# Kernel tuning notes

Measured on AMD Instinct MI355X. Metric: run time of the kernel, lower is better.

## Reference

```python
import jax, jax.numpy as jnp
import numpy as np

N_DOMAINS = 8
BATCH, SEQ, VOCAB = 4, 2048, 32000


def setup_inputs() -> dict:
    key = jax.random.key(0)
    k1, k2, k3 = jax.random.split(key, 3)
    sharded_logits = jax.random.normal(k1, (BATCH, SEQ, VOCAB), dtype=jnp.float32)
    label_ids = jax.random.randint(k2, (BATCH, SEQ), 0, VOCAB, dtype=jnp.int64)
    label_mask = jnp.ones((BATCH, SEQ), dtype=bool)
    domain_idxs = jax.random.randint(k3, (BATCH,), 0, N_DOMAINS, dtype=jnp.int64)
    return {"sharded_logits": sharded_logits, "label_ids": label_ids,
            "label_mask": label_mask, "domain_idxs": domain_idxs}


def reference(sharded_logits, label_ids, label_mask, domain_idxs):
    # sharded_cross_entropy(dtype=float): per-token -log p(label), computed in fp32
    logp = jax.nn.log_softmax(sharded_logits.astype(jnp.float32), axis=-1)
    per_token_loss = -jnp.take_along_axis(logp, label_ids[..., None], axis=-1)[..., 0]  # [B, S]

    # masked_mean
    mask = label_mask.astype(jnp.float32)
    ce_loss = jnp.sum(per_token_loss * mask) / jnp.sum(mask)

    # per-domain loss: vectorized segment-sum replaces the python for-loop scatter-add
    per_sample_loss = per_token_loss.sum(axis=-1)                                  # [B]
    domain_losses = jax.ops.segment_sum(per_sample_loss, domain_idxs,
                                        num_segments=N_DOMAINS)                    # [D]
    samples_per_domain = jnp.bincount(domain_idxs, length=N_DOMAINS)               # [D]
    seq_len = per_token_loss.shape[1]
    denom = (samples_per_domain * seq_len).astype(jnp.float32)
    # divide then zero-out NaNs (empty domains) == torch's isnan -> 0 fixup
    normalized = jnp.where(denom > 0, domain_losses / jnp.maximum(denom, 1.0), 0.0)
    return ce_loss, normalized, samples_per_domain
```

## Files before the change

### kernel.cpp

```cpp
#include <hip/hip_runtime.h>
#include <hip/hip_bf16.h>
#include <math.h>


#define NDOM 8

typedef float v4f __attribute__((ext_vector_type(4)));
typedef int   v4i __attribute__((ext_vector_type(4)));

__global__ __launch_bounds__(256) void ce_per_token_kernel(
    const float* __restrict__ logits,
    const int* __restrict__ labels,
    float* __restrict__ per_token_loss,
    int V)
{
    const int token = blockIdx.x;
    const int t = threadIdx.x;
    const v4f* row = reinterpret_cast<const v4f*>(logits + (size_t)token * (size_t)V);
    const int V4 = V >> 2;
    const float L2E = 1.4426950408889634f;
    const float LN2 = 0.6931471805599453f;

    float m[4]  = {-INFINITY, -INFINITY, -INFINITY, -INFINITY};
    float mL[4] = {0.f, 0.f, 0.f, 0.f};
    float s[4]  = {0.f, 0.f, 0.f, 0.f};

    auto upd = [&](int k, v4f v) {
        float m4 = fmaxf(fmaxf(v.x, v.y), fmaxf(v.z, v.w));
        if (m4 > m[k]) {
            s[k] *= exp2f((m[k] - m4) * L2E);
            m[k] = m4;
            mL[k] = m4 * L2E;
        }
        s[k] += exp2f(fmaf(v.x, L2E, -mL[k])) + exp2f(fmaf(v.y, L2E, -mL[k]))
              + exp2f(fmaf(v.z, L2E, -mL[k])) + exp2f(fmaf(v.w, L2E, -mL[k]));
    };

    int j = t;
    for (; j + 768 < V4; j += 1024) {
        v4f v0 = __builtin_nontemporal_load(row + j);
        v4f v1 = __builtin_nontemporal_load(row + j + 256);
        v4f v2 = __builtin_nontemporal_load(row + j + 512);
        v4f v3 = __builtin_nontemporal_load(row + j + 768);
        upd(0, v0); upd(1, v1); upd(2, v2); upd(3, v3);
    }
    for (; j < V4; j += 256) {
        v4f v = __builtin_nontemporal_load(row + j);
        upd(0, v);
    }

    float M = m[0], S = s[0];
    #pragma unroll
    for (int k = 1; k < 4; k++) {
        float mn = fmaxf(M, m[k]);
        S = S * exp2f((M - mn) * L2E) + s[k] * exp2f((m[k] - mn) * L2E);
        M = mn;
    }

    #pragma unroll
    for (int off = 1; off < 64; off <<= 1) {
        float mo = __shfl_xor(M, off, 64);
        float so = __shfl_xor(S, off, 64);
        float mn = fmaxf(M, mo);
        S = S * exp2f((M - mn) * L2E) + so * exp2f((mo - mn) * L2E);
        M = mn;
    }

    __shared__ float sm[4];
    __shared__ float ss[4];
    const int wave = t >> 6;
    if ((t & 63) == 0) { sm[wave] = M; ss[wave] = S; }
    __syncthreads();

    if (t == 0) {
        float Mf = fmaxf(fmaxf(sm[0], sm[1]), fmaxf(sm[2], sm[3]));
        float Sf = ss[0] * exp2f((sm[0] - Mf) * L2E) + ss[1] * exp2f((sm[1] - Mf) * L2E)
                 + ss[2] * exp2f((sm[2] - Mf) * L2E) + ss[3] * exp2f((sm[3] - Mf) * L2E);
        int lab = labels[token];
        float x = logits[(size_t)token * (size_t)V + (size_t)lab];
        per_token_loss[token] = Mf + log2f(Sf) * LN2 - x;
    }
}

__global__ __launch_bounds__(256) void ce_finalize_kernel(
    const float* __restrict__ per_token_loss,
    const int* __restrict__ mask,
    const int* __restrict__ domain_idxs,
    float* __restrict__ out,
    int T, int B, int S)
{
    const int t = threadIdx.x;
    const v4f* pl4 = reinterpret_cast<const v4f*>(per_token_loss);
    const v4i* mk4 = reinterpret_cast<const v4i*>(mask);
    const int T4 = T >> 2;
    const int S4 = S >> 2;

    float tot = 0.0f, cnt = 0.0f;
    float samp[4] = {0.f, 0.f, 0.f, 0.f};

    for (int i = t; i < T4; i += 256) {
        v4f l = pl4[i];
        v4i mk = mk4[i];
        tot += (mk.x ? l.x : 0.f) + (mk.y ? l.y : 0.f)
             + (mk.z ? l.z : 0.f) + (mk.w ? l.w : 0.f);
        cnt += (mk.x ? 1.f : 0.f) + (mk.y ? 1.f : 0.f)
             + (mk.z ? 1.f : 0.f) + (mk.w ? 1.f : 0.f);
        samp[i / S4] += l.x + l.y + l.z + l.w;
    }

    __shared__ float red[6][256];
    red[0][t] = tot;     red[1][t] = cnt;
    red[2][t] = samp[0]; red[3][t] = samp[1];
    red[4][t] = samp[2]; red[5][t] = samp[3];
    __syncthreads();

    for (int off = 128; off > 0; off >>= 1) {
        if (t < off) {
            #pragma unroll
            for (int k = 0; k < 6; k++) red[k][t] += red[k][t + off];
        }
        __syncthreads();
    }

    if (t == 0) {
        out[0] = red[0][0] / red[1][0];

        float dl[NDOM];
        int sc[NDOM];
        #pragma unroll
        for (int d = 0; d < NDOM; d++) { dl[d] = 0.0f; sc[d] = 0; }
        for (int b = 0; b < B; b++) {
            int d = domain_idxs[b];
            dl[d] += red[2 + b][0];
            sc[d] += 1;
        }
        #pragma unroll
        for (int d = 0; d < NDOM; d++) {
            float denom = (float)sc[d] * (float)S;
            out[1 + d]        = (denom > 0.0f) ? (dl[d] / denom) : 0.0f;
            out[1 + NDOM + d] = (float)sc[d];
        }
    }
}

extern "C" void kernel_launch(void* const* d_in, const int* in_sizes, int n_in,
                              void* d_out, int out_size, void* d_ws, size_t ws_size,
                              hipStream_t stream) {
    const float* logits     = (const float*)d_in[0];
    const int* labels       = (const int*)d_in[1];
    const int* mask         = (const int*)d_in[2];
    const int* domain_idxs  = (const int*)d_in[3];
    float* out              = (float*)d_out;

    const int T = in_sizes[1];
    const int V = in_sizes[0] / T;
    const int B = in_sizes[3];
    const int S = T / B;

    float* per_token_loss = (float*)d_ws;

    ce_per_token_kernel<<<T, 256, 0, stream>>>(logits, labels, per_token_loss, V);
    ce_finalize_kernel<<<1, 256, 0, stream>>>(per_token_loss, mask, domain_idxs,
                                              out, T, B, S);
}
```

Before: 1.261 ms.

## Assign one wave per row with register double-buffered loads

```diff
diff --git a/kernel.cpp b/kernel.cpp
--- a/kernel.cpp
+++ b/kernel.cpp
@@ -1,5 +1,4 @@
 #include <hip/hip_runtime.h>
-#include <hip/hip_bf16.h>
 #include <math.h>
 
 
@@ -8,22 +7,30 @@
 typedef float v4f __attribute__((ext_vector_type(4)));
 typedef int   v4i __attribute__((ext_vector_type(4)));
 
-__global__ __launch_bounds__(256) void ce_per_token_kernel(
+__global__ __launch_bounds__(256) void ce_rowwave_kernel(
     const float* __restrict__ logits,
     const int* __restrict__ labels,
     float* __restrict__ per_token_loss,
     int V)
 {
-    const int token = blockIdx.x;
-    const int t = threadIdx.x;
-    const v4f* row = reinterpret_cast<const v4f*>(logits + (size_t)token * (size_t)V);
-    const int V4 = V >> 2;
+    const int lane = threadIdx.x & 63;
+    const int row  = (blockIdx.x << 2) + (threadIdx.x >> 6);
+
     const float L2E = 1.4426950408889634f;
     const float LN2 = 0.6931471805599453f;
 
-    float m[4]  = {-INFINITY, -INFINITY, -INFINITY, -INFINITY};
-    float mL[4] = {0.f, 0.f, 0.f, 0.f};
-    float s[4]  = {0.f, 0.f, 0.f, 0.f};
+    const size_t rowbase = (size_t)row * (size_t)V;
+    const v4f* rp = reinterpret_cast<const v4f*>(logits + rowbase);
+    const int V4     = V >> 2;
+    const int nchunk = V4 >> 6;
+    const int nfull  = nchunk / 5;
+
+    const int   lab = labels[row];
+    const float xl  = logits[rowbase + (size_t)lab];
+
+    float m[5]  = {-INFINITY, -INFINITY, -INFINITY, -INFINITY, -INFINITY};
+    float mL[5] = {0.f, 0.f, 0.f, 0.f, 0.f};
+    float s[5]  = {0.f, 0.f, 0.f, 0.f, 0.f};
 
     auto upd = [&](int k, v4f v) {
         float m4 = fmaxf(fmaxf(v.x, v.y), fmaxf(v.z, v.w));
@@ -36,22 +43,33 @@
               + exp2f(fmaf(v.z, L2E, -mL[k])) + exp2f(fmaf(v.w, L2E, -mL[k]));
     };
 
-    int j = t;
-    for (; j + 768 < V4; j += 1024) {
-        v4f v0 = __builtin_nontemporal_load(row + j);
-        v4f v1 = __builtin_nontemporal_load(row + j + 256);
-        v4f v2 = __builtin_nontemporal_load(row + j + 512);
-        v4f v3 = __builtin_nontemporal_load(row + j + 768);
-        upd(0, v0); upd(1, v1); upd(2, v2); upd(3, v3);
+    v4f cur[5], nxt[5];
+    #pragma unroll
+    for (int c = 0; c < 5; ++c)
+        cur[c] = __builtin_nontemporal_load(rp + (c << 6) + lane);
+
+    for (int i = 1; i < nfull; ++i) {
+        const int base = i * 320 + lane;
+        #pragma unroll
+        for (int c = 0; c < 5; ++c)
+            nxt[c] = __builtin_nontemporal_load(rp + base + (c << 6));
+        #pragma unroll
+        for (int c = 0; c < 5; ++c)
+            upd(c, cur[c]);
+        #pragma unroll
+        for (int c = 0; c < 5; ++c)
+            cur[c] = nxt[c];
     }
-    for (; j < V4; j += 256) {
-        v4f v = __builtin_nontemporal_load(row + j);
-        upd(0, v);
-    }
+    #pragma unroll
+    for (int c = 0; c < 5; ++c)
+        upd(c, cur[c]);
+
+    for (int k = nfull * 5; k < nchunk; ++k)
+        upd(0, __builtin_nontemporal_load(rp + (k << 6) + lane));
 
     float M = m[0], S = s[0];
     #pragma unroll
-    for (int k = 1; k < 4; k++) {
+    for (int k = 1; k < 5; ++k) {
         float mn = fmaxf(M, m[k]);
         S = S * exp2f((M - mn) * L2E) + s[k] * exp2f((m[k] - mn) * L2E);
         M = mn;
@@ -66,20 +84,8 @@
         M = mn;
     }
 
-    __shared__ float sm[4];
-    __shared__ float ss[4];
-    const int wave = t >> 6;
-    if ((t & 63) == 0) { sm[wave] = M; ss[wave] = S; }
-    __syncthreads();
-
-    if (t == 0) {
-        float Mf = fmaxf(fmaxf(sm[0], sm[1]), fmaxf(sm[2], sm[3]));
-        float Sf = ss[0] * exp2f((sm[0] - Mf) * L2E) + ss[1] * exp2f((sm[1] - Mf) * L2E)
-                 + ss[2] * exp2f((sm[2] - Mf) * L2E) + ss[3] * exp2f((sm[3] - Mf) * L2E);
-        int lab = labels[token];
-        float x = logits[(size_t)token * (size_t)V + (size_t)lab];
-        per_token_loss[token] = Mf + log2f(Sf) * LN2 - x;
-    }
+    if (lane == 0)
+        per_token_loss[row] = M + log2f(S) * LN2 - xl;
 }
 
 __global__ __launch_bounds__(256) void ce_finalize_kernel(
@@ -159,7 +165,7 @@
 
     float* per_token_loss = (float*)d_ws;
 
-    ce_per_token_kernel<<<T, 256, 0, stream>>>(logits, labels, per_token_loss, V);
+    ce_rowwave_kernel<<<T >> 2, 256, 0, stream>>>(logits, labels, per_token_loss, V);
     ce_finalize_kernel<<<1, 256, 0, stream>>>(per_token_loss, mask, domain_idxs,
                                               out, T, B, S);
 }
```

Measured after the change: 1.263 ms. No clear change (+0.2%).
